# Kernel tuning notes

Hardware: AMD Instinct MI355X
Metric: run time of the kernel (lower is better)

Reference implementation:

```python
import jax, jax.numpy as jnp
import numpy as np

B, T, E, H = 512, 256, 384, 64

def setup_inputs() -> dict:
    key = jax.random.key(0)
    k1, k2, k3, k4 = jax.random.split(key, 4)
    scale = 1.0 / np.sqrt(E)
    return {
        "x":  jax.random.normal(k1, (B, T, E), dtype=jnp.float32),
        "Wq": jax.random.normal(k2, (E, H), dtype=jnp.float32) * scale,
        "Wk": jax.random.normal(k3, (E, H), dtype=jnp.float32) * scale,
        "Wv": jax.random.normal(k4, (E, H), dtype=jnp.float32) * scale,
    }

def reference(x, Wq, Wk, Wv):
    # single-head causal self-attention (dropout in eval mode / identity)
    q = jnp.einsum('bte,eh->bth', x, Wq)
    k = jnp.einsum('bte,eh->bth', x, Wk)
    v = jnp.einsum('bte,eh->bth', x, Wv)
    d = q.shape[-1]
    wei = jnp.einsum('bqh,bkh->bqk', q, k) * (d ** -0.5)   # [B,T,T]
    T_ = x.shape[1]
    causal = jnp.tril(jnp.ones((T_, T_), dtype=bool))
    wei = jnp.where(causal[None, :, :], wei, -jnp.inf)
    wei = jax.nn.softmax(wei, axis=-1)
    out = jnp.einsum('bqk,bkh->bqh', wei, v)               # [B,T,H]
    return out
```

## Files before the change

### kernel.cpp

```cpp
#include <hip/hip_runtime.h>

typedef __attribute__((ext_vector_type(4)))  float f32x4;
typedef __attribute__((ext_vector_type(16))) float f32x16;
typedef __attribute__((ext_vector_type(8)))  short s16x8;


__device__ inline short f2bf(float f){
  unsigned u = __float_as_uint(f);
  u = u + 0x7fffu + ((u >> 16) & 1u);
  return (short)(u >> 16);
}

__global__ void wt_prep_kernel(const float* __restrict__ Wq, const float* __restrict__ Wk,
                               const float* __restrict__ Wv, short* __restrict__ Wt){
  int o = blockIdx.x * 256 + threadIdx.x;
  if (o >= 192*384) return;
  int n = o / 384, k = o - n*384;
  const float* W = (n < 64) ? Wq : (n < 128) ? Wk : Wv;
  Wt[o] = f2bf(W[k*64 + (n & 63)]);
}

__global__ __launch_bounds__(256) void proj_kernel(const float* __restrict__ x, const short* __restrict__ Wt,
                            short* __restrict__ Q, short* __restrict__ K, short* __restrict__ Vt){
  __shared__ __align__(16) short Bt[192*72];
  const int tid  = threadIdx.x;
  const int wave = tid >> 6, lane = tid & 63;
  const int l31  = lane & 31, hh = lane >> 5;
  const long row0  = (long)blockIdx.x * 128;
  const long myrow = row0 + wave*32 + l31;

  f32x16 acc[6];
  #pragma unroll
  for (int c = 0; c < 6; ++c)
    #pragma unroll
    for (int j = 0; j < 16; ++j) acc[c][j] = 0.0f;

  for (int kt = 0; kt < 6; ++kt){
    const int k0 = kt*64;
    #pragma unroll
    for (int i = 0; i < 6; ++i){
      int c = tid + i*256;
      int n = c >> 3, co = (c & 7) * 8;
      s16x8 wv = *(const s16x8*)(Wt + n*384 + k0 + co);
      *(s16x8*)(Bt + n*72 + co) = wv;
    }
    __syncthreads();
    #pragma unroll
    for (int s = 0; s < 4; ++s){
      const float* xp = x + myrow*384 + (k0 + s*16 + hh*8);
      float4 a0 = *(const float4*)xp;
      float4 a1 = *(const float4*)(xp + 4);
      s16x8 af;
      af[0]=f2bf(a0.x); af[1]=f2bf(a0.y); af[2]=f2bf(a0.z); af[3]=f2bf(a0.w);
      af[4]=f2bf(a1.x); af[5]=f2bf(a1.y); af[6]=f2bf(a1.z); af[7]=f2bf(a1.w);
      #pragma unroll
      for (int c = 0; c < 6; ++c){
        s16x8 bfr = *(const s16x8*)(Bt + (c*32 + l31)*72 + s*16 + hh*8);
        acc[c] = __builtin_amdgcn_mfma_f32_32x32x16_bf16(af, bfr, acc[c], 0, 0, 0);
      }
    }
    __syncthreads();
  }
  #pragma unroll
  for (int c = 0; c < 6; ++c){
    const int n = c*32 + l31;
    #pragma unroll
    for (int reg = 0; reg < 16; ++reg){
      const int  rowC = (reg & 3) + 8*(reg >> 2) + 4*hh;
      const long r    = row0 + wave*32 + rowC;
      const short v   = f2bf(acc[c][reg]);
      if (n < 64)       Q[r*64 + n] = v;
      else if (n < 128) K[r*64 + (n - 64)] = v;
      else              Vt[(r >> 8)*16384 + (long)(n - 128)*256 + (r & 255)] = v;
    }
  }
}

__global__ __launch_bounds__(256) void attn_kernel(const short* __restrict__ Q, const short* __restrict__ K,
                            const short* __restrict__ Vt, float* __restrict__ out){
  __shared__ __align__(16) short P[4][16*40];
  const int tid  = threadIdx.x;
  const int w    = tid >> 6, lane = tid & 63;
  const int l15  = lane & 15, quad = lane >> 4;
  const int b    = blockIdx.x >> 2, qt = blockIdx.x & 3;
  const int qbase = qt*64 + w*16;
  const int NFw  = (qbase >> 4) + 1;
  const int NSw  = (NFw + 1) >> 1;

  const short* Qs = Q  + ((long)b*256 + qbase)*64;
  const short* Ks = K  + (long)b*256*64;
  const short* Vs = Vt + (long)b*64*256;

  s16x8 qf0 = *(const s16x8*)(Qs + l15*64 + quad*8);
  s16x8 qf1 = *(const s16x8*)(Qs + l15*64 + 32 + quad*8);

  f32x4 sc[16];
  #pragma unroll
  for (int f = 0; f < 16; ++f){
    f32x4 a;
    #pragma unroll
    for (int r = 0; r < 4; ++r) a[r] = 0.0f;
    if (f < NFw){
      const short* kp = Ks + (f*16 + l15)*64 + quad*8;
      s16x8 k0v = *(const s16x8*)kp;
      s16x8 k1v = *(const s16x8*)(kp + 32);
      a = __builtin_amdgcn_mfma_f32_16x16x32_bf16(qf0, k0v, a, 0, 0, 0);
      a = __builtin_amdgcn_mfma_f32_16x16x32_bf16(qf1, k1v, a, 0, 0, 0);
    }
    sc[f] = a;
  }

  float mx[4], sm[4];
  #pragma unroll
  for (int r = 0; r < 4; ++r) mx[r] = -3.0e38f;
  #pragma unroll
  for (int f = 0; f < 16; ++f){
    if (f < NFw){
      const int key = f*16 + l15;
      #pragma unroll
      for (int r = 0; r < 4; ++r){
        const int qg = qbase + quad*4 + r;
        float s = sc[f][r] * 0.125f;
        s = (key <= qg) ? s : -1.0e30f;
        sc[f][r] = s;
        mx[r] = fmaxf(mx[r], s);
      }
    }
  }
  #pragma unroll
  for (int r = 0; r < 4; ++r){
    #pragma unroll
    for (int off = 1; off < 16; off <<= 1) mx[r] = fmaxf(mx[r], __shfl_xor(mx[r], off, 16));
  }
  #pragma unroll
  for (int r = 0; r < 4; ++r) sm[r] = 0.0f;
  #pragma unroll
  for (int f = 0; f < 16; ++f){
    if (f < NFw){
      #pragma unroll
      for (int r = 0; r < 4; ++r){
        float p = exp2f((sc[f][r] - mx[r]) * 1.44269504f);
        sc[f][r] = p;
        sm[r] += p;
      }
    }
  }
  #pragma unroll
  for (int r = 0; r < 4; ++r){
    #pragma unroll
    for (int off = 1; off < 16; off <<= 1) sm[r] += __shfl_xor(sm[r], off, 16);
  }

  f32x4 o[4];
  #pragma unroll
  for (int h = 0; h < 4; ++h)
    #pragma unroll
    for (int r = 0; r < 4; ++r) o[h][r] = 0.0f;

  short* Pw = P[w];
  #pragma unroll
  for (int ks = 0; ks < 8; ++ks){
    if (ks < NSw){
      #pragma unroll
      for (int fi = 0; fi < 2; ++fi){
        const int f = 2*ks + fi;
        #pragma unroll
        for (int r = 0; r < 4; ++r){
          short v = 0;
          if (f < NFw) v = f2bf(sc[f][r]);
          Pw[(quad*4 + r)*40 + fi*16 + l15] = v;
        }
      }
      s16x8 pf = *(const s16x8*)(Pw + l15*40 + quad*8);
      #pragma unroll
      for (int h = 0; h < 4; ++h){
        s16x8 vf = *(const s16x8*)(Vs + (h*16 + l15)*256 + ks*32 + quad*8);
        o[h] = __builtin_amdgcn_mfma_f32_16x16x32_bf16(pf, vf, o[h], 0, 0, 0);
      }
    }
  }

  float* op = out + ((long)b*256 + qbase)*64;
  #pragma unroll
  for (int r = 0; r < 4; ++r){
    const float inv = 1.0f / sm[r];
    #pragma unroll
    for (int h = 0; h < 4; ++h)
      op[(quad*4 + r)*64 + h*16 + l15] = o[h][r] * inv;
  }
}

extern "C" void kernel_launch(void* const* d_in, const int* in_sizes, int n_in,
                              void* d_out, int out_size, void* d_ws, size_t ws_size,
                              hipStream_t stream){
  const float* x  = (const float*)d_in[0];
  const float* Wq = (const float*)d_in[1];
  const float* Wk = (const float*)d_in[2];
  const float* Wv = (const float*)d_in[3];
  float* out = (float*)d_out;

  char* ws = (char*)d_ws;
  short* Wt = (short*)ws;
  short* Q  = (short*)(ws + 147456);
  short* K  = (short*)(ws + 147456 + 16777216);
  short* Vt = (short*)(ws + 147456 + 2*16777216);

  hipLaunchKernelGGL(wt_prep_kernel, dim3(288),  dim3(256), 0, stream, Wq, Wk, Wv, Wt);
  hipLaunchKernelGGL(proj_kernel,    dim3(1024), dim3(256), 0, stream, x, Wt, Q, K, Vt);
  hipLaunchKernelGGL(attn_kernel,    dim3(2048), dim3(256), 0, stream, Q, K, Vt, out);
}
```

Before: 389.6 us.

## Fuse QKV projection and causal attention into one per-batch kernel using LDS

Merges the projection and attention kernels into a single kernel with one 512-thread block per batch. Q, K and transposed V are kept in shared memory instead of being written to and re-read from global memory. Weight fragments are now read straight from global/L2 rather than staged through LDS, with x supplied as the B operand. Each wave handles a pair of query tiles (w and 15-w) to balance the causal workload. The cost is heavy LDS use (~112KB), which limits occupancy to about one or two blocks per CU, and a grid of only 512 blocks.

```diff
diff --git a/kernel.cpp b/kernel.cpp
--- a/kernel.cpp
+++ b/kernel.cpp
@@ -3,6 +3,7 @@
 typedef __attribute__((ext_vector_type(4)))  float f32x4;
 typedef __attribute__((ext_vector_type(16))) float f32x16;
 typedef __attribute__((ext_vector_type(8)))  short s16x8;
+typedef __attribute__((ext_vector_type(4)))  short s16x4;
 
 
 __device__ inline short f2bf(float f){
@@ -20,14 +21,19 @@
   Wt[o] = f2bf(W[k*64 + (n & 63)]);
 }
 
-__global__ __launch_bounds__(256) void proj_kernel(const float* __restrict__ x, const short* __restrict__ Wt,
-                            short* __restrict__ Q, short* __restrict__ K, short* __restrict__ Vt){
-  __shared__ __align__(16) short Bt[192*72];
+__global__ __launch_bounds__(512, 2) void fused_kernel(const float* __restrict__ x,
+                             const short* __restrict__ Wt, float* __restrict__ out){
+  __shared__ __align__(16) short Qs[256*72];
+  __shared__ __align__(16) short Ks[256*72];
+  __shared__ __align__(16) short Vts[64*264];
+  __shared__ __align__(16) short Pp[8][16*40];
+
   const int tid  = threadIdx.x;
-  const int wave = tid >> 6, lane = tid & 63;
+  const int w    = tid >> 6, lane = tid & 63;
   const int l31  = lane & 31, hh = lane >> 5;
-  const long row0  = (long)blockIdx.x * 128;
-  const long myrow = row0 + wave*32 + l31;
+  const int b    = blockIdx.x;
+
+  const float* xb = x + ((long)b*256 + w*32)*384;
 
   f32x16 acc[6];
   #pragma unroll
@@ -35,158 +41,153 @@
     #pragma unroll
     for (int j = 0; j < 16; ++j) acc[c][j] = 0.0f;
 
+  #pragma unroll 2
   for (int kt = 0; kt < 6; ++kt){
-    const int k0 = kt*64;
-    #pragma unroll
-    for (int i = 0; i < 6; ++i){
-      int c = tid + i*256;
-      int n = c >> 3, co = (c & 7) * 8;
-      s16x8 wv = *(const s16x8*)(Wt + n*384 + k0 + co);
-      *(s16x8*)(Bt + n*72 + co) = wv;
-    }
-    __syncthreads();
     #pragma unroll
     for (int s = 0; s < 4; ++s){
-      const float* xp = x + myrow*384 + (k0 + s*16 + hh*8);
+      const int k0 = kt*64 + s*16 + hh*8;
+      const float* xp = xb + l31*384 + k0;
       float4 a0 = *(const float4*)xp;
       float4 a1 = *(const float4*)(xp + 4);
-      s16x8 af;
-      af[0]=f2bf(a0.x); af[1]=f2bf(a0.y); af[2]=f2bf(a0.z); af[3]=f2bf(a0.w);
-      af[4]=f2bf(a1.x); af[5]=f2bf(a1.y); af[6]=f2bf(a1.z); af[7]=f2bf(a1.w);
+      s16x8 bx;
+      bx[0]=f2bf(a0.x); bx[1]=f2bf(a0.y); bx[2]=f2bf(a0.z); bx[3]=f2bf(a0.w);
+      bx[4]=f2bf(a1.x); bx[5]=f2bf(a1.y); bx[6]=f2bf(a1.z); bx[7]=f2bf(a1.w);
       #pragma unroll
       for (int c = 0; c < 6; ++c){
-        s16x8 bfr = *(const s16x8*)(Bt + (c*32 + l31)*72 + s*16 + hh*8);
-        acc[c] = __builtin_amdgcn_mfma_f32_32x32x16_bf16(af, bfr, acc[c], 0, 0, 0);
-      }
-    }
-    __syncthreads();
+        s16x8 wa = *(const s16x8*)(Wt + (c*32 + l31)*384 + k0);
+        acc[c] = __builtin_amdgcn_mfma_f32_32x32x16_bf16(wa, bx, acc[c], 0, 0, 0);
+      }
+    }
+  }
+
+  const int trow = w*32 + l31;
+  #pragma unroll
+  for (int c = 0; c < 4; ++c){
+    short* dst = (c < 2) ? Qs : Ks;
+    const int nb = (c & 1)*32;
+    #pragma unroll
+    for (int g = 0; g < 4; ++g){
+      s16x4 v;
+      #pragma unroll
+      for (int i = 0; i < 4; ++i) v[i] = f2bf(acc[c][g*4 + i]);
+      *(s16x4*)(dst + trow*72 + nb + 8*g + 4*hh) = v;
+    }
   }
   #pragma unroll
-  for (int c = 0; c < 6; ++c){
-    const int n = c*32 + l31;
+  for (int c = 4; c < 6; ++c)
     #pragma unroll
     for (int reg = 0; reg < 16; ++reg){
-      const int  rowC = (reg & 3) + 8*(reg >> 2) + 4*hh;
-      const long r    = row0 + wave*32 + rowC;
-      const short v   = f2bf(acc[c][reg]);
-      if (n < 64)       Q[r*64 + n] = v;
-      else if (n < 128) K[r*64 + (n - 64)] = v;
-      else              Vt[(r >> 8)*16384 + (long)(n - 128)*256 + (r & 255)] = v;
-    }
-  }
-}
-
-__global__ __launch_bounds__(256) void attn_kernel(const short* __restrict__ Q, const short* __restrict__ K,
-                            const short* __restrict__ Vt, float* __restrict__ out){
-  __shared__ __align__(16) short P[4][16*40];
-  const int tid  = threadIdx.x;
-  const int w    = tid >> 6, lane = tid & 63;
-  const int l15  = lane & 15, quad = lane >> 4;
-  const int b    = blockIdx.x >> 2, qt = blockIdx.x & 3;
-  const int qbase = qt*64 + w*16;
-  const int NFw  = (qbase >> 4) + 1;
-  const int NSw  = (NFw + 1) >> 1;
-
-  const short* Qs = Q  + ((long)b*256 + qbase)*64;
-  const short* Ks = K  + (long)b*256*64;
-  const short* Vs = Vt + (long)b*64*256;
-
-  s16x8 qf0 = *(const s16x8*)(Qs + l15*64 + quad*8);
-  s16x8 qf1 = *(const s16x8*)(Qs + l15*64 + 32 + quad*8);
-
-  f32x4 sc[16];
-  #pragma unroll
-  for (int f = 0; f < 16; ++f){
-    f32x4 a;
-    #pragma unroll
-    for (int r = 0; r < 4; ++r) a[r] = 0.0f;
-    if (f < NFw){
-      const short* kp = Ks + (f*16 + l15)*64 + quad*8;
-      s16x8 k0v = *(const s16x8*)kp;
-      s16x8 k1v = *(const s16x8*)(kp + 32);
-      a = __builtin_amdgcn_mfma_f32_16x16x32_bf16(qf0, k0v, a, 0, 0, 0);
-      a = __builtin_amdgcn_mfma_f32_16x16x32_bf16(qf1, k1v, a, 0, 0, 0);
-    }
-    sc[f] = a;
-  }
-
-  float mx[4], sm[4];
-  #pragma unroll
-  for (int r = 0; r < 4; ++r) mx[r] = -3.0e38f;
-  #pragma unroll
-  for (int f = 0; f < 16; ++f){
-    if (f < NFw){
-      const int key = f*16 + l15;
-      #pragma unroll
-      for (int r = 0; r < 4; ++r){
-        const int qg = qbase + quad*4 + r;
-        float s = sc[f][r] * 0.125f;
-        s = (key <= qg) ? s : -1.0e30f;
-        sc[f][r] = s;
-        mx[r] = fmaxf(mx[r], s);
-      }
-    }
-  }
-  #pragma unroll
-  for (int r = 0; r < 4; ++r){
-    #pragma unroll
-    for (int off = 1; off < 16; off <<= 1) mx[r] = fmaxf(mx[r], __shfl_xor(mx[r], off, 16));
-  }
-  #pragma unroll
-  for (int r = 0; r < 4; ++r) sm[r] = 0.0f;
-  #pragma unroll
-  for (int f = 0; f < 16; ++f){
-    if (f < NFw){
-      #pragma unroll
-      for (int r = 0; r < 4; ++r){
-        float p = exp2f((sc[f][r] - mx[r]) * 1.44269504f);
-        sc[f][r] = p;
-        sm[r] += p;
-      }
-    }
-  }
-  #pragma unroll
-  for (int r = 0; r < 4; ++r){
-    #pragma unroll
-    for (int off = 1; off < 16; off <<= 1) sm[r] += __shfl_xor(sm[r], off, 16);
-  }
-
-  f32x4 o[4];
-  #pragma unroll
-  for (int h = 0; h < 4; ++h)
-    #pragma unroll
-    for (int r = 0; r < 4; ++r) o[h][r] = 0.0f;
-
-  short* Pw = P[w];
-  #pragma unroll
-  for (int ks = 0; ks < 8; ++ks){
-    if (ks < NSw){
-      #pragma unroll
-      for (int fi = 0; fi < 2; ++fi){
-        const int f = 2*ks + fi;
+      const int h = (c-4)*32 + (reg & 3) + 8*(reg >> 2) + 4*hh;
+      Vts[h*264 + trow] = f2bf(acc[c][reg]);
+    }
+
+  __syncthreads();
+
+  const int l15 = lane & 15, quad = lane >> 4;
+  float* ob = out + (long)b*256*64;
+  short* Pw = Pp[w];
+
+  for (int it = 0; it < 2; ++it){
+    const int F  = it ? (15 - w) : w;
+    const int qb = F*16;
+    const int NF = F + 1;
+    const int NS = (NF + 1) >> 1;
+
+    s16x8 qf0 = *(const s16x8*)(Qs + (qb + l15)*72 + quad*8);
+    s16x8 qf1 = *(const s16x8*)(Qs + (qb + l15)*72 + 32 + quad*8);
+
+    f32x4 sc[16];
+    #pragma unroll
+    for (int f = 0; f < 16; ++f){
+      f32x4 a;
+      #pragma unroll
+      for (int r = 0; r < 4; ++r) a[r] = 0.0f;
+      if (f < NF){
+        const short* kp = Ks + (f*16 + l15)*72 + quad*8;
+        s16x8 k0v = *(const s16x8*)kp;
+        s16x8 k1v = *(const s16x8*)(kp + 32);
+        a = __builtin_amdgcn_mfma_f32_16x16x32_bf16(qf0, k0v, a, 0, 0, 0);
+        a = __builtin_amdgcn_mfma_f32_16x16x32_bf16(qf1, k1v, a, 0, 0, 0);
+      }
+      sc[f] = a;
+    }
+
+    float mx[4], sm[4];
+    #pragma unroll
+    for (int r = 0; r < 4; ++r) mx[r] = -3.0e38f;
+    #pragma unroll
+    for (int f = 0; f < 16; ++f){
+      if (f < NF){
+        const int key = f*16 + l15;
         #pragma unroll
         for (int r = 0; r < 4; ++r){
-          short v = 0;
-          if (f < NFw) v = f2bf(sc[f][r]);
-          Pw[(quad*4 + r)*40 + fi*16 + l15] = v;
-        }
-      }
-      s16x8 pf = *(const s16x8*)(Pw + l15*40 + quad*8);
-      #pragma unroll
-      for (int h = 0; h < 4; ++h){
-        s16x8 vf = *(const s16x8*)(Vs + (h*16 + l15)*256 + ks*32 + quad*8);
-        o[h] = __builtin_amdgcn_mfma_f32_16x16x32_bf16(pf, vf, o[h], 0, 0, 0);
-      }
-    }
-  }
-
-  float* op = out + ((long)b*256 + qbase)*64;
-  #pragma unroll
-  for (int r = 0; r < 4; ++r){
-    const float inv = 1.0f / sm[r];
-    #pragma unroll
-    for (int h = 0; h < 4; ++h)
-      op[(quad*4 + r)*64 + h*16 + l15] = o[h][r] * inv;
+          const int qg = qb + quad*4 + r;
+          float s = sc[f][r] * 0.125f;
+          s = (key <= qg) ? s : -1.0e30f;
+          sc[f][r] = s;
+          mx[r] = fmaxf(mx[r], s);
+        }
+      }
+    }
+    #pragma unroll
+    for (int r = 0; r < 4; ++r){
+      #pragma unroll
+      for (int off = 1; off < 16; off <<= 1) mx[r] = fmaxf(mx[r], __shfl_xor(mx[r], off, 16));
+    }
+    #pragma unroll
+    for (int r = 0; r < 4; ++r) sm[r] = 0.0f;
+    #pragma unroll
+    for (int f = 0; f < 16; ++f){
+      if (f < NF){
+        #pragma unroll
+        for (int r = 0; r < 4; ++r){
+          float p = exp2f((sc[f][r] - mx[r]) * 1.44269504f);
+          sc[f][r] = p;
+          sm[r] += p;
+        }
+      }
+    }
+    #pragma unroll
+    for (int r = 0; r < 4; ++r){
+      #pragma unroll
+      for (int off = 1; off < 16; off <<= 1) sm[r] += __shfl_xor(sm[r], off, 16);
+    }
+
+    f32x4 o[4];
+    #pragma unroll
+    for (int h0 = 0; h0 < 4; ++h0)
+      #pragma unroll
+      for (int r = 0; r < 4; ++r) o[h0][r] = 0.0f;
+
+    #pragma unroll
+    for (int ks = 0; ks < 8; ++ks){
+      if (ks < NS){
+        #pragma unroll
+        for (int fi = 0; fi < 2; ++fi){
+          const int f = 2*ks + fi;
+          #pragma unroll
+          for (int r = 0; r < 4; ++r){
+            short v = 0;
+            if (f < NF) v = f2bf(sc[f][r]);
+            Pw[(quad*4 + r)*40 + fi*16 + l15] = v;
+          }
+        }
+        s16x8 pf = *(const s16x8*)(Pw + l15*40 + quad*8);
+        #pragma unroll
+        for (int h0 = 0; h0 < 4; ++h0){
+          s16x8 vf = *(const s16x8*)(Vts + (h0*16 + l15)*264 + ks*32 + quad*8);
+          o[h0] = __builtin_amdgcn_mfma_f32_16x16x32_bf16(pf, vf, o[h0], 0, 0, 0);
+        }
+      }
+    }
+
+    #pragma unroll
+    for (int r = 0; r < 4; ++r){
+      const float inv = 1.0f / sm[r];
+      #pragma unroll
+      for (int h0 = 0; h0 < 4; ++h0)
+        ob[(qb + quad*4 + r)*64 + h0*16 + l15] = o[h0][r] * inv;
+    }
   }
 }
 
@@ -199,13 +200,8 @@
   const float* Wv = (const float*)d_in[3];
   float* out = (float*)d_out;
 
-  char* ws = (char*)d_ws;
-  short* Wt = (short*)ws;
-  short* Q  = (short*)(ws + 147456);
-  short* K  = (short*)(ws + 147456 + 16777216);
-  short* Vt = (short*)(ws + 147456 + 2*16777216);
-
-  hipLaunchKernelGGL(wt_prep_kernel, dim3(288),  dim3(256), 0, stream, Wq, Wk, Wv, Wt);
-  hipLaunchKernelGGL(proj_kernel,    dim3(1024), dim3(256), 0, stream, x, Wt, Q, K, Vt);
-  hipLaunchKernelGGL(attn_kernel,    dim3(2048), dim3(256), 0, stream, Q, K, Vt, out);
-}
+  short* Wt = (short*)d_ws;
+
+  hipLaunchKernelGGL(wt_prep_kernel, dim3(288), dim3(256), 0, stream, Wq, Wk, Wv, Wt);
+  hipLaunchKernelGGL(fused_kernel,   dim3(512), dim3(512), 0, stream, x, Wt, out);
+}
```

After: 361.8 us. 1.08x faster.

## Restructure projection GEMM: drop LDS staging, swap operands, split outputs across waves

Applied to the files above, without the earlier changes.

The projection kernel no longer stages weights in shared memory with block barriers. Each wave now reads bf16 weight fragments straight from global memory, where they are likely to hit in L2, and register-prefetches the next x slice. Operands are swapped so the weights form the A matrix, which lets Q and K be written as contiguous 4-element vector stores. Work is split so each block covers 64 rows, with wave pairs each handling 96 output columns, giving twice as many blocks and 3 accumulators per wave instead of 6, with launch bounds tuned for occupancy. The trade-off is that weight fragments are reloaded from cache by every wave and x is read twice per row.

```diff
diff --git a/kernel.cpp b/kernel.cpp
--- a/kernel.cpp
+++ b/kernel.cpp
@@ -3,6 +3,7 @@
 typedef __attribute__((ext_vector_type(4)))  float f32x4;
 typedef __attribute__((ext_vector_type(16))) float f32x16;
 typedef __attribute__((ext_vector_type(8)))  short s16x8;
+typedef __attribute__((ext_vector_type(4)))  short s16x4;
 
 
 __device__ inline short f2bf(float f){
@@ -20,58 +21,62 @@
   Wt[o] = f2bf(W[k*64 + (n & 63)]);
 }
 
-__global__ __launch_bounds__(256) void proj_kernel(const float* __restrict__ x, const short* __restrict__ Wt,
-                            short* __restrict__ Q, short* __restrict__ K, short* __restrict__ Vt){
-  __shared__ __align__(16) short Bt[192*72];
+__global__ __launch_bounds__(256, 4) void proj_kernel(const float* __restrict__ x,
+                            const short* __restrict__ Wt,
+                            short* __restrict__ Q, short* __restrict__ K,
+                            short* __restrict__ Vt){
   const int tid  = threadIdx.x;
-  const int wave = tid >> 6, lane = tid & 63;
+  const int w    = tid >> 6, lane = tid & 63;
   const int l31  = lane & 31, hh = lane >> 5;
-  const long row0  = (long)blockIdx.x * 128;
-  const long myrow = row0 + wave*32 + l31;
-
-  f32x16 acc[6];
-  #pragma unroll
-  for (int c = 0; c < 6; ++c)
-    #pragma unroll
-    for (int j = 0; j < 16; ++j) acc[c][j] = 0.0f;
-
-  for (int kt = 0; kt < 6; ++kt){
-    const int k0 = kt*64;
-    #pragma unroll
-    for (int i = 0; i < 6; ++i){
-      int c = tid + i*256;
-      int n = c >> 3, co = (c & 7) * 8;
-      s16x8 wv = *(const s16x8*)(Wt + n*384 + k0 + co);
-      *(s16x8*)(Bt + n*72 + co) = wv;
-    }
-    __syncthreads();
-    #pragma unroll
-    for (int s = 0; s < 4; ++s){
-      const float* xp = x + myrow*384 + (k0 + s*16 + hh*8);
-      float4 a0 = *(const float4*)xp;
-      float4 a1 = *(const float4*)(xp + 4);
-      s16x8 af;
-      af[0]=f2bf(a0.x); af[1]=f2bf(a0.y); af[2]=f2bf(a0.z); af[3]=f2bf(a0.w);
-      af[4]=f2bf(a1.x); af[5]=f2bf(a1.y); af[6]=f2bf(a1.z); af[7]=f2bf(a1.w);
-      #pragma unroll
-      for (int c = 0; c < 6; ++c){
-        s16x8 bfr = *(const s16x8*)(Bt + (c*32 + l31)*72 + s*16 + hh*8);
-        acc[c] = __builtin_amdgcn_mfma_f32_32x32x16_bf16(af, bfr, acc[c], 0, 0, 0);
-      }
-    }
-    __syncthreads();
-  }
-  #pragma unroll
-  for (int c = 0; c < 6; ++c){
-    const int n = c*32 + l31;
-    #pragma unroll
-    for (int reg = 0; reg < 16; ++reg){
-      const int  rowC = (reg & 3) + 8*(reg >> 2) + 4*hh;
-      const long r    = row0 + wave*32 + rowC;
-      const short v   = f2bf(acc[c][reg]);
-      if (n < 64)       Q[r*64 + n] = v;
-      else if (n < 128) K[r*64 + (n - 64)] = v;
-      else              Vt[(r >> 8)*16384 + (long)(n - 128)*256 + (r & 255)] = v;
+  const int ch   = (w & 1) * 96;
+  const long trow = (long)blockIdx.x*64 + (w >> 1)*32 + l31;
+  const float* xp = x + trow*384 + hh*8;
+
+  f32x16 acc[3];
+  #pragma unroll
+  for (int c = 0; c < 3; ++c)
+    #pragma unroll
+    for (int q = 0; q < 16; ++q) acc[c][q] = 0.0f;
+
+  float4 c0 = *(const float4*)xp;
+  float4 c1 = *(const float4*)(xp + 4);
+  #pragma unroll
+  for (int s = 0; s < 24; ++s){
+    float4 n0, n1;
+    if (s < 23){
+      n0 = *(const float4*)(xp + (s+1)*16);
+      n1 = *(const float4*)(xp + (s+1)*16 + 4);
+    }
+    s16x8 bx;
+    bx[0]=f2bf(c0.x); bx[1]=f2bf(c0.y); bx[2]=f2bf(c0.z); bx[3]=f2bf(c0.w);
+    bx[4]=f2bf(c1.x); bx[5]=f2bf(c1.y); bx[6]=f2bf(c1.z); bx[7]=f2bf(c1.w);
+    #pragma unroll
+    for (int c = 0; c < 3; ++c){
+      s16x8 wa = *(const s16x8*)(Wt + (ch + c*32 + l31)*384 + s*16 + hh*8);
+      acc[c] = __builtin_amdgcn_mfma_f32_32x32x16_bf16(wa, bx, acc[c], 0, 0, 0);
+    }
+    c0 = n0; c1 = n1;
+  }
+
+  #pragma unroll
+  for (int c = 0; c < 3; ++c){
+    const int n0 = ch + c*32;
+    if (n0 < 128){
+      short* dst = (n0 < 64) ? (Q + trow*64 + n0) : (K + trow*64 + (n0 - 64));
+      #pragma unroll
+      for (int g = 0; g < 4; ++g){
+        s16x4 v;
+        #pragma unroll
+        for (int i = 0; i < 4; ++i) v[i] = f2bf(acc[c][g*4 + i]);
+        *(s16x4*)(dst + 8*g + 4*hh) = v;
+      }
+    } else {
+      short* vb = Vt + (trow >> 8)*16384 + (trow & 255);
+      #pragma unroll
+      for (int reg = 0; reg < 16; ++reg){
+        const int h = (n0 - 128) + (reg & 3) + 8*(reg >> 2) + 4*hh;
+        vb[h*256] = f2bf(acc[c][reg]);
+      }
     }
   }
 }
@@ -206,6 +211,6 @@
   short* Vt = (short*)(ws + 147456 + 2*16777216);
 
   hipLaunchKernelGGL(wt_prep_kernel, dim3(288),  dim3(256), 0, stream, Wq, Wk, Wv, Wt);
-  hipLaunchKernelGGL(proj_kernel,    dim3(1024), dim3(256), 0, stream, x, Wt, Q, K, Vt);
+  hipLaunchKernelGGL(proj_kernel,    dim3(2048), dim3(256), 0, stream, x, Wt, Q, K, Vt);
   hipLaunchKernelGGL(attn_kernel,    dim3(2048), dim3(256), 0, stream, Q, K, Vt, out);
 }
```

After: 469.0 us. 20.4% more time.
